# Performance work log

Hardware: AMD Instinct MI355X
Metric: run time of the kernel (lower is better)

## Reference

```python
import jax, jax.numpy as jnp
import numpy as np

DN = ('NCHW', 'OIHW', 'NCHW')

def conv(x, w, b=None, pad='SAME'):
    y = jax.lax.conv_general_dilated(x, w, (1, 1), pad, dimension_numbers=DN)
    if b is not None:
        y = y + b[None, :, None, None]
    return y

def prelu(x, a):
    return jnp.where(x >= 0, x, a * x)

def ca_layer(x, w_a, w_b):
    # global avg pool -> 1x1 conv -> relu -> 1x1 conv -> sigmoid -> gate
    g = jnp.mean(x, axis=(2, 3), keepdims=True)          # [B,C,1,1]
    g = jax.nn.relu(conv(g, w_a))
    g = jax.nn.sigmoid(conv(g, w_b))
    return x * g

def head(x, w, b, ca_a, ca_b):
    y = conv(x, w, b)                                    # [B,4,H,W]
    y = ca_layer(y, ca_a, ca_b)
    return jax.nn.softmax(y, axis=1)                     # Softmax2d = softmax over C

def box_kernel(k):
    return jnp.full((1, 1, k, k), 1.0 / (k * k), dtype=jnp.float32)

def multiscale_blur(x):
    # SAME-padded uniform box filters of sizes 1,5,15,25 on [B,1,H,W]
    return [x if k == 1 else conv(x, box_kernel(k)) for k in (1, 5, 15, 25)]

def weighted_combine(h, blurs):
    # h: [B,4,H,W] softmax weights; blurs: list of 4 [B,1,H,W]
    return sum(h[:, i:i+1] * blurs[i] for i in range(4))

def setup_inputs() -> dict:
    key = jax.random.key(0)
    ks = jax.random.split(key, 32)
    B, H, W = 8, 512, 512
    s = 0.05
    inp = {
        'x':  jax.random.normal(ks[0], (B, 1, H, W), jnp.float32),
        'w1': jax.random.normal(ks[1], (32, 1, 3, 3), jnp.float32) * s,
        'b1': jnp.zeros((32,), jnp.float32),
        'a1': jnp.float32(0.25),
        'w2': jax.random.normal(ks[2], (64, 32, 3, 3), jnp.float32) * s,
        'b2': jnp.zeros((64,), jnp.float32),
        'a2': jnp.float32(0.25),
        'w3': jax.random.normal(ks[3], (32, 64, 3, 3), jnp.float32) * s,
        'b3': jnp.zeros((32,), jnp.float32),
        'a3': jnp.float32(0.25),
    }
    for i, kk in zip((1, 2, 3), (4, 8, 12)):
        inp[f'hw{i}'] = jax.random.normal(ks[kk], (4, 32, 3, 3), jnp.float32) * s
        inp[f'hb{i}'] = jnp.zeros((4,), jnp.float32)
        inp[f'ca{i}a'] = jax.random.normal(ks[kk + 1], (4, 4, 1, 1), jnp.float32) * s
        inp[f'ca{i}b'] = jax.random.normal(ks[kk + 2], (4, 4, 1, 1), jnp.float32) * s
    return inp

def reference(x, w1, b1, a1, w2, b2, a2, w3, b3, a3,
              hw1, hb1, ca1a, ca1b, hw2, hb2, ca2a, ca2b, hw3, hb3, ca3a, ca3b):
    body = prelu(conv(x, w1, b1), a1)
    body = prelu(conv(body, w2, b2), a2)
    body = prelu(conv(body, w3, b3), a3)            # [B,32,H,W]
    h1 = head(body, hw1, hb1, ca1a, ca1b)
    h2 = head(body, hw2, hb2, ca2a, ca2b)
    h3 = head(body, hw3, hb3, ca3a, ca3b)
    out1 = weighted_combine(h1, multiscale_blur(x))
    out2 = weighted_combine(h2, multiscale_blur(out1))
    out3 = weighted_combine(h3, multiscale_blur(out2))
    return out3
```

## Files before the change

### kernel.cpp

```cpp
#include <hip/hip_runtime.h>

#define HH 512
#define WW 512
#define NB 8
#define HWSZ (HH * WW)
#define PW 516
#define PROWS 514

typedef float f32x4 __attribute__((ext_vector_type(4)));
typedef float f32x16 __attribute__((ext_vector_type(16)));
typedef short bf16x8 __attribute__((ext_vector_type(8)));

__device__ __forceinline__ unsigned short f2bf(float f) {
  union { float f; unsigned u; } v; v.f = f;
  unsigned r = v.u + 0x7FFFu + ((v.u >> 16) & 1u);
  return (unsigned short)(r >> 16);
}
__device__ __forceinline__ float bf2f(unsigned u16) {
  union { unsigned u; float f; } v; v.u = u16 << 16;
  return v.f;
}

__device__ __forceinline__ void gload16(const uint4* g, uint4* l) {
  __builtin_amdgcn_global_load_lds((__attribute__((address_space(1))) void*)g,
                                   (__attribute__((address_space(3))) void*)l, 16, 0, 0);
}

#define PS1 ((size_t)PROWS * PW * 32)
#define PS2 ((size_t)PROWS * PW * 64)
#define NZ1 (2 * 4 * PW * 8 + 512 * 4 * 16)
#define NZ2 (2 * 8 * PW * 8 + 512 * 8 * 16)

__device__ __forceinline__ void zp(unsigned short* buf, int NCH, int i) {
  int rowShorts = NCH * PW * 8;
  if (i < 2 * rowShorts) {
    size_t r = (i < rowShorts) ? 0 : 513;
    int j = i % rowShorts;
    buf[r * rowShorts + j] = 0;
    return;
  }
  i -= 2 * rowShorts;
  int perRow = NCH * 16;
  int r = 1 + i / perRow;
  int j = i % perRow;
  int ch = j >> 4;
  int c = (j & 8) ? 513 : 0;
  int e = j & 7;
  buf[(((size_t)r * NCH + ch) * PW + c) * 8 + e] = 0;
}

__global__ __launch_bounds__(256) void k_prep(const float* __restrict__ w2,
                                              const float* __restrict__ w3,
                                              const float* __restrict__ h0,
                                              const float* __restrict__ h1,
                                              const float* __restrict__ h2,
                                              unsigned short* __restrict__ wp2,
                                              unsigned short* __restrict__ wp3,
                                              unsigned short* __restrict__ wph,
                                              unsigned short* __restrict__ t1,
                                              unsigned short* __restrict__ t2,
                                              float* __restrict__ S) {
  int i = blockIdx.x * 256 + threadIdx.x;
  const int N1 = 9 * 64 * 32;
  const int N2 = N1 + 9 * 32 * 64;
  const int N3 = N2 + 9 * 16 * 32;
  const int N4 = N3 + 4 * NZ1;
  const int N5 = N4 + 4 * NZ2;
  const int N6 = N5 + 128;
  if (i < N1) {
    int j8 = i & 7;
    int lane = (i >> 3) & 63;
    int mt = (i >> 9) & 1;
    int ks = (i >> 10) & 1;
    int tap = i >> 11;
    int l31 = lane & 31, h16 = lane >> 5;
    int oc = mt * 32 + l31;
    int ic = ks * 16 + h16 * 8 + j8;
    wp2[i] = f2bf(w2[(oc * 32 + ic) * 9 + tap]);
  } else if (i < N2) {
    int j = i - N1;
    int ic = j & 63, t = j >> 6, oc = t & 31, k = t >> 5;
    wp3[j] = f2bf(w3[(oc * 64 + ic) * 9 + k]);
  } else if (i < N3) {
    int j = i - N2;
    int ic = j & 31, t = j >> 5, oc = t & 15, k = t >> 4;
    float v = 0.f;
    if (oc < 12) {
      const float* w = oc < 4 ? h0 : (oc < 8 ? h1 : h2);
      v = w[((oc & 3) * 32 + ic) * 9 + k];
    }
    wph[j] = f2bf(v);
  } else if (i < N4) {
    int j = i - N3;
    zp(t1 + (size_t)(j / NZ1) * PS1, 4, j % NZ1);
  } else if (i < N5) {
    int j = i - N4;
    zp(t2 + (size_t)(j / NZ2) * PS2, 8, j % NZ2);
  } else if (i < N6) {
    S[i - N5] = 0.f;
  }
}

__global__ __launch_bounds__(256) void k_conv1(const float* __restrict__ x,
                                               const float* __restrict__ w,
                                               const float* __restrict__ bias,
                                               const float* __restrict__ a_ptr,
                                               unsigned short* __restrict__ out) {
  const float* xp = x + (size_t)blockIdx.z * HWSZ;
  uint4* out4 = (uint4*)(out + (size_t)blockIdx.z * PS1);
  int pix = blockIdx.x * 256 + threadIdx.x;
  int h = pix >> 9, wc = pix & 511;
  float t[9];
#pragma unroll
  for (int dh = 0; dh < 3; dh++)
#pragma unroll
    for (int dw = 0; dw < 3; dw++) {
      int hh = h + dh - 1, ww = wc + dw - 1;
      t[dh * 3 + dw] =
          (hh >= 0 && hh < HH && ww >= 0 && ww < WW) ? xp[hh * WW + ww] : 0.f;
    }
  float a = a_ptr[0];
  unsigned pk[16];
#pragma unroll
  for (int oc = 0; oc < 32; oc++) {
    float s = bias[oc];
#pragma unroll
    for (int k = 0; k < 9; k++) s = fmaf(w[oc * 9 + k], t[k], s);
    s = s >= 0.f ? s : a * s;
    unsigned short b = f2bf(s);
    if (oc & 1)
      pk[oc >> 1] |= ((unsigned)b) << 16;
    else
      pk[oc >> 1] = b;
  }
#pragma unroll
  for (int q = 0; q < 4; q++)
    out4[((size_t)(h + 1) * 4 + q) * PW + (wc + 1)] = *(uint4*)&pk[q * 4];
}

__global__ __launch_bounds__(256, 2) void k_convm2(const unsigned short* __restrict__ in,
                                                   const unsigned short* __restrict__ wp,
                                                   const float* __restrict__ bias,
                                                   const float* __restrict__ a_ptr,
                                                   unsigned short* __restrict__ out) {
  __shared__ __align__(16) short ring[10 * 4 * 68 * 8];
  __shared__ __align__(16) short wlds[9 * 2 * 2 * 64 * 8];
  const int tid = threadIdx.x, lane = tid & 63, wid = tid >> 6;
  const int l31 = lane & 31, h16 = lane >> 5;
  const int c0 = blockIdx.x * 64;
  const int R0 = blockIdx.y * 32;
  const uint4* in4 = (const uint4*)(in + (size_t)blockIdx.z * PS1);
  unsigned short* outz = out + (size_t)blockIdx.z * PS2;
  uint4* ring4 = (uint4*)ring;
  uint4* wl4 = (uint4*)wlds;
  const uint4* wp4 = (const uint4*)wp;

  for (int sg = wid; sg < 36; sg += 4)
    gload16(wp4 + sg * 64 + lane, wl4 + sg * 64);

  auto load_rows = [&](int rfirst, int nrows) {
    int nseg = nrows * 4;
    for (int sg = wid; sg < nseg; sg += 4) {
      int rr = rfirst + (sg >> 2);
      int ch = sg & 3;
      const uint4* src = in4 + (size_t)(rr * 4 + ch) * PW + c0;
      uint4* dst = ring4 + ((rr % 10) * 4 + ch) * 68;
      gload16(src + lane, dst);
      gload16(src + 4 + lane, dst + 4);
    }
  };

  const float alpha = a_ptr[0];
  load_rows(R0, 6);

  for (int k = 0; k < 8; ++k) {
    const int rb = R0 + 4 * k;
    __syncthreads();
    if (k < 7) load_rows(rb + 6, 4);

    f32x16 acc[2][2];
#pragma unroll
    for (int nt = 0; nt < 2; nt++)
#pragma unroll
      for (int mt = 0; mt < 2; mt++)
#pragma unroll
        for (int j = 0; j < 16; j++) acc[nt][mt][j] = 0.f;

#pragma unroll
    for (int dh = 0; dh < 3; dh++) {
      bf16x8 af[3][2][2];
#pragma unroll
      for (int dw = 0; dw < 3; dw++)
#pragma unroll
        for (int ks = 0; ks < 2; ks++)
#pragma unroll
          for (int mt = 0; mt < 2; mt++)
            af[dw][ks][mt] = *(const bf16x8*)(
                wlds + ((((size_t)((dh * 3 + dw) * 2 + ks) * 2 + mt) * 64 + lane) * 8));
      const short* lrow = ring + (size_t)(((rb + wid + dh) % 10) * 4) * 68 * 8;
#pragma unroll
      for (int dw = 0; dw < 3; dw++) {
        const int pl0 = l31 + dw, pl1 = 32 + l31 + dw;
#pragma unroll
        for (int ks = 0; ks < 2; ks++) {
          const int blk = ks * 2 + h16;
          bf16x8 b0 = *(const bf16x8*)(lrow + (blk * 68 + pl0) * 8);
          bf16x8 b1 = *(const bf16x8*)(lrow + (blk * 68 + pl1) * 8);
#pragma unroll
          for (int mt = 0; mt < 2; mt++)
            acc[0][mt] = __builtin_amdgcn_mfma_f32_32x32x16_bf16(af[dw][ks][mt],
                                                                 b0, acc[0][mt], 0, 0, 0);
#pragma unroll
          for (int mt = 0; mt < 2; mt++)
            acc[1][mt] = __builtin_amdgcn_mfma_f32_32x32x16_bf16(af[dw][ks][mt],
                                                                 b1, acc[1][mt], 0, 0, 0);
        }
      }
    }

    const int orow = rb + wid + 1;
    uint2* o2 = (uint2*)outz;
#pragma unroll
    for (int nt = 0; nt < 2; nt++) {
      const int ocol = c0 + nt * 32 + l31 + 1;
#pragma unroll
      for (int mt = 0; mt < 2; mt++)
#pragma unroll
        for (int g = 0; g < 4; g++) {
          int oc0 = mt * 32 + g * 8 + h16 * 4;
          f32x4 bv = *(const f32x4*)(bias + oc0);
          float v[4];
#pragma unroll
          for (int j = 0; j < 4; j++) {
            float s = acc[nt][mt][g * 4 + j] + bv[j];
            v[j] = s >= 0.f ? s : alpha * s;
          }
          uint2 pk;
          pk.x = (unsigned)f2bf(v[0]) | ((unsigned)f2bf(v[1]) << 16);
          pk.y = (unsigned)f2bf(v[2]) | ((unsigned)f2bf(v[3]) << 16);
          size_t idx16 = ((size_t)orow * 8 + (mt * 4 + g)) * PW + ocol;
          o2[idx16 * 2 + h16] = pk;
        }
    }
  }
}

__global__ __launch_bounds__(256, 2) void k_convm3(const unsigned short* __restrict__ in,
                                                   const unsigned short* __restrict__ wp,
                                                   const float* __restrict__ bias,
                                                   const float* __restrict__ a_ptr,
                                                   unsigned short* __restrict__ out) {
  __shared__ __align__(16) short lds[8 * 8 * 68 * 8];
  const int tid = threadIdx.x, lane = tid & 63, wid = tid >> 6;
  const int l31 = lane & 31, h16 = lane >> 5;
  const int c0 = blockIdx.x * 64;
  const int R0 = blockIdx.y * 32;
  const uint4* in4 = (const uint4*)(in + (size_t)blockIdx.z * PS2);
  unsigned short* outz = out + (size_t)blockIdx.z * PS1;
  uint4* lds4 = (uint4*)lds;

  bf16x8 af[9][4];
#pragma unroll
  for (int k9 = 0; k9 < 9; k9++)
#pragma unroll
    for (int ks = 0; ks < 4; ks++)
      af[k9][ks] = *(const bf16x8*)(
          wp + ((size_t)(k9 * 32 + l31) * 64 + ks * 16 + h16 * 8));

  auto load_rows = [&](int rfirst, int nrows) {
    int nseg = nrows * 8;
    for (int sg = wid; sg < nseg; sg += 4) {
      int rr = rfirst + (sg >> 3);
      int ch = sg & 7;
      const uint4* src = in4 + (size_t)(rr * 8 + ch) * PW + c0;
      uint4* dst = lds4 + ((rr & 7) * 8 + ch) * 68;
      gload16(src + lane, dst);
      gload16(src + 4 + lane, dst + 4);
    }
  };

  const float alpha = a_ptr[0];
  load_rows(R0, 6);

  for (int k = 0; k < 8; ++k) {
    const int rb = R0 + 4 * k;
    __syncthreads();
    if (k < 7) load_rows(rb + 6, 2);

    f32x16 acc[2];
#pragma unroll
    for (int nt = 0; nt < 2; nt++)
#pragma unroll
      for (int j = 0; j < 16; j++) acc[nt][j] = 0.f;

#pragma unroll
    for (int dh = 0; dh < 3; dh++) {
      const short* lrow = lds + (size_t)(((rb + wid + dh) & 7) * 8) * 68 * 8;
#pragma unroll
      for (int dw = 0; dw < 3; dw++) {
        const int pl0 = l31 + dw, pl1 = 32 + l31 + dw;
#pragma unroll
        for (int ks = 0; ks < 4; ks++) {
          const int blk = ks * 2 + h16;
          bf16x8 b0 = *(const bf16x8*)(lrow + (blk * 68 + pl0) * 8);
          bf16x8 b1 = *(const bf16x8*)(lrow + (blk * 68 + pl1) * 8);
          acc[0] = __builtin_amdgcn_mfma_f32_32x32x16_bf16(af[dh * 3 + dw][ks],
                                                           b0, acc[0], 0, 0, 0);
          acc[1] = __builtin_amdgcn_mfma_f32_32x32x16_bf16(af[dh * 3 + dw][ks],
                                                           b1, acc[1], 0, 0, 0);
        }
      }
    }

    const int orow = rb + wid + 1;
    uint2* o2 = (uint2*)outz;
#pragma unroll
    for (int nt = 0; nt < 2; nt++) {
      const int ocol = c0 + nt * 32 + l31 + 1;
#pragma unroll
      for (int g = 0; g < 4; g++) {
        int oc0 = g * 8 + h16 * 4;
        f32x4 bv = *(const f32x4*)(bias + oc0);
        float v[4];
#pragma unroll
        for (int j = 0; j < 4; j++) {
          float s = acc[nt][g * 4 + j] + bv[j];
          v[j] = s >= 0.f ? s : alpha * s;
        }
        uint2 pk;
        pk.x = (unsigned)f2bf(v[0]) | ((unsigned)f2bf(v[1]) << 16);
        pk.y = (unsigned)f2bf(v[2]) | ((unsigned)f2bf(v[3]) << 16);
        size_t idx16 = ((size_t)orow * 4 + g) * PW + ocol;
        o2[idx16 * 2 + h16] = pk;
      }
    }
    __syncthreads();
    if (k < 7) load_rows(rb + 8, 2);
  }
}

__global__ __launch_bounds__(256, 2) void k_headm(const unsigned short* __restrict__ in,
                                                  const unsigned short* __restrict__ wp,
                                                  const float* __restrict__ hb0,
                                                  const float* __restrict__ hb1,
                                                  const float* __restrict__ hb2,
                                                  unsigned short* __restrict__ pre,
                                                  float* __restrict__ S) {
  __shared__ __align__(16) short lds[8 * 4 * 68 * 8];
  __shared__ float part[4][4][4];
  const int tid = threadIdx.x, lane = tid & 63, wid = tid >> 6;
  const int l15 = lane & 15, q = lane >> 4;
  const int c0 = blockIdx.x * 64;
  const int R0 = blockIdx.y * 32;
  const uint4* in4 = (const uint4*)(in + (size_t)blockIdx.z * PS1);
  float* Sz = S + blockIdx.z * 16;
  uint4* lds4 = (uint4*)lds;

  bf16x8 af[9];
#pragma unroll
  for (int k9 = 0; k9 < 9; k9++)
    af[k9] = *(const bf16x8*)(wp + (size_t)(k9 * 16 + l15) * 32 + q * 8);

  float bs[4];
#pragma unroll
  for (int r = 0; r < 4; r++) {
    int oc = q * 4 + r;
    bs[r] = oc < 4 ? hb0[oc] : (oc < 8 ? hb1[oc - 4] : (oc < 12 ? hb2[oc - 8] : 0.f));
  }
  unsigned short* prehq = pre + ((size_t)(q * 4 + blockIdx.z) * HWSZ) * 4;

  auto load_rows = [&](int rfirst, int nrows) {
    int nseg = nrows * 4;
    for (int sg = wid; sg < nseg; sg += 4) {
      int rr = rfirst + (sg >> 2);
      int ch = sg & 3;
      const uint4* src = in4 + (size_t)(rr * 4 + ch) * PW + c0;
      uint4* dst = lds4 + ((rr & 7) * 4 + ch) * 68;
      gload16(src + lane, dst);
      gload16(src + 4 + lane, dst + 4);
    }
  };

  load_rows(R0, 6);
  float csum[4] = {0.f, 0.f, 0.f, 0.f};

  for (int k = 0; k < 8; ++k) {
    const int rb = R0 + 4 * k;
    __syncthreads();
    if (k < 7) load_rows(rb + 6, 2);

    f32x4 acc[4];
#pragma unroll
    for (int nt = 0; nt < 4; nt++)
#pragma unroll
      for (int j = 0; j < 4; j++) acc[nt][j] = 0.f;

#pragma unroll
    for (int dh = 0; dh < 3; dh++) {
      const short* lrow = lds + (size_t)(((rb + wid + dh) & 7) * 4) * 68 * 8;
#pragma unroll
      for (int dw = 0; dw < 3; dw++) {
        bf16x8 a = af[dh * 3 + dw];
#pragma unroll
        for (int nt = 0; nt < 4; nt++) {
          int pl = nt * 16 + l15 + dw;
          bf16x8 b = *(const bf16x8*)(lrow + (q * 68 + pl) * 8);
          acc[nt] = __builtin_amdgcn_mfma_f32_16x16x32_bf16(a, b, acc[nt], 0, 0, 0);
        }
      }
    }

    const int orow = rb + wid;
#pragma unroll
    for (int nt = 0; nt < 4; nt++) {
      int pix = orow * 512 + c0 + nt * 16 + l15;
      float v[4];
#pragma unroll
      for (int r = 0; r < 4; r++) {
        v[r] = acc[nt][r] + bs[r];
        csum[r] += v[r];
      }
      uint2 pk;
      pk.x = (unsigned)f2bf(v[0]) | ((unsigned)f2bf(v[1]) << 16);
      pk.y = (unsigned)f2bf(v[2]) | ((unsigned)f2bf(v[3]) << 16);
      *(uint2*)(prehq + (size_t)pix * 4) = pk;
    }
    __syncthreads();
    if (k < 7) load_rows(rb + 8, 2);
  }

#pragma unroll
  for (int d = 1; d < 16; d <<= 1)
#pragma unroll
    for (int r = 0; r < 4; r++) csum[r] += __shfl_xor(csum[r], d, 64);
  if (l15 == 0)
#pragma unroll
    for (int r = 0; r < 4; r++) part[wid][q][r] = csum[r];
  __syncthreads();
  if (tid < 12) {
    int oc = tid;
    float s = part[0][oc >> 2][oc & 3] + part[1][oc >> 2][oc & 3] +
              part[2][oc >> 2][oc & 3] + part[3][oc >> 2][oc & 3];
    atomicAdd(&Sz[oc], s);
  }
}

#define BT 32
#define RAD 12
#define SRCT (BT + 2 * RAD)
__global__ __launch_bounds__(256) void k_blurcombine(const float* __restrict__ src,
                                                     const unsigned short* __restrict__ preh,
                                                     const float* __restrict__ S4,
                                                     const float* __restrict__ wa,
                                                     const float* __restrict__ wb,
                                                     float* __restrict__ dst) {
  __shared__ float tile[SRCT][SRCT];
  __shared__ float hs[3][SRCT][BT];
  __shared__ float g[4];
  const float* srcz = src + (size_t)blockIdx.z * HWSZ;
  const unsigned short* prez = preh + (size_t)blockIdx.z * HWSZ * 4;
  const float* S4z = S4 + blockIdx.z * 16;
  float* dstz = dst + (size_t)blockIdx.z * HWSZ;
  int h0 = blockIdx.y * BT - RAD, w0 = blockIdx.x * BT - RAD;
  if (threadIdx.x < 4) {
    int o = threadIdx.x;
    float m[4], ga[4];
#pragma unroll
    for (int c = 0; c < 4; c++) m[c] = S4z[c] * (1.0f / (float)HWSZ);
#pragma unroll
    for (int c = 0; c < 4; c++) {
      float s = 0.f;
#pragma unroll
      for (int j = 0; j < 4; j++) s = fmaf(wa[c * 4 + j], m[j], s);
      ga[c] = fmaxf(s, 0.f);
    }
    float s2 = 0.f;
#pragma unroll
    for (int c = 0; c < 4; c++) s2 = fmaf(wb[o * 4 + c], ga[c], s2);
    g[o] = 1.f / (1.f + expf(-s2));
  }
  for (int idx = threadIdx.x; idx < SRCT * SRCT; idx += 256) {
    int r = idx / SRCT, c = idx % SRCT;
    int hh = h0 + r, ww = w0 + c;
    float v = 0.f;
    if (hh >= 0 && hh < HH && ww >= 0 && ww < WW) v = srcz[hh * WW + ww];
    tile[r][c] = v;
  }
  __syncthreads();
  for (int idx = threadIdx.x; idx < SRCT * BT; idx += 256) {
    int r = idx / BT, j = idx % BT;
    int cc = j + RAD;
    float s5 = 0.f;
#pragma unroll
    for (int d = -2; d <= 2; d++) s5 += tile[r][cc + d];
    float s15 = s5;
#pragma unroll
    for (int d = 3; d <= 7; d++) s15 += tile[r][cc + d] + tile[r][cc - d];
    float s25 = s15;
#pragma unroll
    for (int d = 8; d <= 12; d++) s25 += tile[r][cc + d] + tile[r][cc - d];
    hs[0][r][j] = s5;
    hs[1][r][j] = s15;
    hs[2][r][j] = s25;
  }
  __syncthreads();
  for (int p = threadIdx.x; p < BT * BT; p += 256) {
    int i = p / BT, j = p % BT;
    int rr = i + RAD;
    float b1 = 0.f;
#pragma unroll
    for (int d = -2; d <= 2; d++) b1 += hs[0][rr + d][j];
    float b2 = 0.f;
#pragma unroll
    for (int d = -7; d <= 7; d++) b2 += hs[1][rr + d][j];
    float b3 = 0.f;
#pragma unroll
    for (int d = -12; d <= 12; d++) b3 += hs[2][rr + d][j];
    b1 *= (1.f / 25.f);
    b2 *= (1.f / 225.f);
    b3 *= (1.f / 625.f);
    float b0 = tile[rr][j + RAD];
    int y = blockIdx.y * BT + i, x = blockIdx.x * BT + j;
    int pix = y * WW + x;
    uint2 pk = *(const uint2*)(prez + (size_t)pix * 4);
    float v[4];
    v[0] = bf2f(pk.x & 0xffffu) * g[0];
    v[1] = bf2f(pk.x >> 16) * g[1];
    v[2] = bf2f(pk.y & 0xffffu) * g[2];
    v[3] = bf2f(pk.y >> 16) * g[3];
    float mx = fmaxf(fmaxf(v[0], v[1]), fmaxf(v[2], v[3]));
    float e0 = expf(v[0] - mx), e1 = expf(v[1] - mx), e2 = expf(v[2] - mx),
          e3 = expf(v[3] - mx);
    float inv = 1.f / (e0 + e1 + e2 + e3);
    dstz[pix] = (e0 * b0 + e1 * b1 + e2 * b2 + e3 * b3) * inv;
  }
}

extern "C" void kernel_launch(void* const* d_in, const int* in_sizes, int n_in,
                              void* d_out, int out_size, void* d_ws, size_t ws_size,
                              hipStream_t stream) {
  const float* x = (const float*)d_in[0];
  const float* w1 = (const float*)d_in[1];
  const float* b1 = (const float*)d_in[2];
  const float* a1 = (const float*)d_in[3];
  const float* w2 = (const float*)d_in[4];
  const float* b2 = (const float*)d_in[5];
  const float* a2 = (const float*)d_in[6];
  const float* w3 = (const float*)d_in[7];
  const float* b3 = (const float*)d_in[8];
  const float* a3 = (const float*)d_in[9];
  const float* hw[3] = {(const float*)d_in[10], (const float*)d_in[14], (const float*)d_in[18]};
  const float* hb[3] = {(const float*)d_in[11], (const float*)d_in[15], (const float*)d_in[19]};
  const float* caa[3] = {(const float*)d_in[12], (const float*)d_in[16], (const float*)d_in[20]};
  const float* cab[3] = {(const float*)d_in[13], (const float*)d_in[17], (const float*)d_in[21]};

  char* base = (char*)d_ws;
  size_t off = 0;
  auto alloc = [&](size_t bytes) {
    char* p = base + off;
    off = (off + bytes + 63) & ~(size_t)63;
    return p;
  };
  unsigned short* t1 = (unsigned short*)alloc(4 * PS1 * 2);
  unsigned short* t2 = (unsigned short*)alloc(4 * PS2 * 2);
  unsigned short* pre = (unsigned short*)alloc(16 * (size_t)HWSZ * 4 * 2);
  unsigned short* wp2 = (unsigned short*)alloc(9 * 64 * 32 * 2);
  unsigned short* wp3 = (unsigned short*)alloc(9 * 64 * 32 * 2);
  unsigned short* wph = (unsigned short*)alloc(9 * 16 * 32 * 2);
  float* out1 = (float*)alloc(4 * (size_t)HWSZ * 4);
  float* out2 = (float*)alloc(4 * (size_t)HWSZ * 4);
  float* S = (float*)alloc(8 * 16 * 4);

  dim3 blk(256);
  {
    int total = 9 * 64 * 32 + 9 * 32 * 64 + 9 * 16 * 32 + 4 * NZ1 + 4 * NZ2 + 128;
    k_prep<<<(total + 255) / 256, blk, 0, stream>>>(w2, w3, hw[0], hw[1], hw[2], wp2,
                                                    wp3, wph, t1, t2, S);
  }

  dim3 gc1(1024, 1, 4);
  dim3 gconv(8, 16, 4);
  dim3 gbc(WW / BT, HH / BT, 4);
  const size_t preplane = (size_t)HWSZ * 4;
  for (int g = 0; g < 2; g++) {
    const float* xg = x + (size_t)g * 4 * HWSZ;
    float* Sg = S + g * 64;
    float* outg = (float*)d_out + (size_t)g * 4 * HWSZ;
    k_conv1<<<gc1, blk, 0, stream>>>(xg, w1, b1, a1, t1);
    k_convm2<<<gconv, blk, 0, stream>>>(t1, wp2, b2, a2, t2);
    k_convm3<<<gconv, blk, 0, stream>>>(t2, wp3, b3, a3, t1);
    k_headm<<<gconv, blk, 0, stream>>>(t1, wph, hb[0], hb[1], hb[2], pre, Sg);
    k_blurcombine<<<gbc, blk, 0, stream>>>(xg, pre + 0 * 4 * preplane, Sg + 0, caa[0], cab[0], out1);
    k_blurcombine<<<gbc, blk, 0, stream>>>(out1, pre + 1 * 4 * preplane, Sg + 4, caa[1], cab[1], out2);
    k_blurcombine<<<gbc, blk, 0, stream>>>(out2, pre + 2 * 4 * preplane, Sg + 8, caa[2], cab[2], outg);
  }
}
```

Baseline: 480.5 us.

## Stage conv3 weights in LDS and halve column tile to cut registers

The third conv kernel no longer keeps all 36 weight fragments in registers. It stages the prepacked weights in shared memory via global_load_lds and reloads 12 fragments per kernel row. The column tile shrinks from 64 to 32, with one accumulator instead of two and a grid doubled in x, and the weight prepack is reordered into a lane-major MFMA fragment layout. The aim is lower register pressure and more blocks in flight, at the cost of extra LDS reads, more halo reloading per output and less weight reuse per block.

```diff
diff --git a/kernel.cpp b/kernel.cpp
--- a/kernel.cpp
+++ b/kernel.cpp
@@ -79,8 +79,13 @@
     wp2[i] = f2bf(w2[(oc * 32 + ic) * 9 + tap]);
   } else if (i < N2) {
     int j = i - N1;
-    int ic = j & 63, t = j >> 6, oc = t & 31, k = t >> 5;
-    wp3[j] = f2bf(w3[(oc * 64 + ic) * 9 + k]);
+    int j8 = j & 7;
+    int lane = (j >> 3) & 63;
+    int ks = (j >> 9) & 3;
+    int tap = j >> 11;
+    int l31 = lane & 31, h16 = lane >> 5;
+    int ic = ks * 16 + h16 * 8 + j8;
+    wp3[j] = f2bf(w3[(l31 * 64 + ic) * 9 + tap]);
   } else if (i < N3) {
     int j = i - N2;
     int ic = j & 31, t = j >> 5, oc = t & 15, k = t >> 4;
@@ -250,22 +255,20 @@
                                                    const float* __restrict__ bias,
                                                    const float* __restrict__ a_ptr,
                                                    unsigned short* __restrict__ out) {
-  __shared__ __align__(16) short lds[8 * 8 * 68 * 8];
+  __shared__ __align__(16) short ring[8 * 8 * 36 * 8];
+  __shared__ __align__(16) short wlds[9 * 4 * 64 * 8];
   const int tid = threadIdx.x, lane = tid & 63, wid = tid >> 6;
   const int l31 = lane & 31, h16 = lane >> 5;
-  const int c0 = blockIdx.x * 64;
+  const int c0 = blockIdx.x * 32;
   const int R0 = blockIdx.y * 32;
   const uint4* in4 = (const uint4*)(in + (size_t)blockIdx.z * PS2);
   unsigned short* outz = out + (size_t)blockIdx.z * PS1;
-  uint4* lds4 = (uint4*)lds;
-
-  bf16x8 af[9][4];
-#pragma unroll
-  for (int k9 = 0; k9 < 9; k9++)
-#pragma unroll
-    for (int ks = 0; ks < 4; ks++)
-      af[k9][ks] = *(const bf16x8*)(
-          wp + ((size_t)(k9 * 32 + l31) * 64 + ks * 16 + h16 * 8));
+  uint4* ring4 = (uint4*)ring;
+  uint4* wl4 = (uint4*)wlds;
+  const uint4* wp4 = (const uint4*)wp;
+
+  for (int sg = wid; sg < 36; sg += 4)
+    gload16(wp4 + sg * 64 + lane, wl4 + sg * 64);
 
   auto load_rows = [&](int rfirst, int nrows) {
     int nseg = nrows * 8;
@@ -273,9 +276,8 @@
       int rr = rfirst + (sg >> 3);
       int ch = sg & 7;
       const uint4* src = in4 + (size_t)(rr * 8 + ch) * PW + c0;
-      uint4* dst = lds4 + ((rr & 7) * 8 + ch) * 68;
-      gload16(src + lane, dst);
-      gload16(src + 4 + lane, dst + 4);
+      uint4* dst = ring4 + ((rr & 7) * 8 + ch) * 36;
+      if (lane < 36) gload16(src + lane, dst);
     }
   };
 
@@ -287,52 +289,50 @@
     __syncthreads();
     if (k < 7) load_rows(rb + 6, 2);
 
-    f32x16 acc[2];
-#pragma unroll
-    for (int nt = 0; nt < 2; nt++)
-#pragma unroll
-      for (int j = 0; j < 16; j++) acc[nt][j] = 0.f;
+    f32x16 acc;
+#pragma unroll
+    for (int j = 0; j < 16; j++) acc[j] = 0.f;
 
 #pragma unroll
     for (int dh = 0; dh < 3; dh++) {
-      const short* lrow = lds + (size_t)(((rb + wid + dh) & 7) * 8) * 68 * 8;
+      bf16x8 af[3][4];
+#pragma unroll
+      for (int dw = 0; dw < 3; dw++)
+#pragma unroll
+        for (int ks = 0; ks < 4; ks++)
+          af[dw][ks] = *(const bf16x8*)(
+              wlds + (((size_t)((dh * 3 + dw) * 4 + ks) * 64 + lane) * 8));
+      const short* lrow = ring + (size_t)(((rb + wid + dh) & 7) * 8) * 36 * 8;
 #pragma unroll
       for (int dw = 0; dw < 3; dw++) {
-        const int pl0 = l31 + dw, pl1 = 32 + l31 + dw;
+        const int pl = l31 + dw;
 #pragma unroll
         for (int ks = 0; ks < 4; ks++) {
           const int blk = ks * 2 + h16;
-          bf16x8 b0 = *(const bf16x8*)(lrow + (blk * 68 + pl0) * 8);
-          bf16x8 b1 = *(const bf16x8*)(lrow + (blk * 68 + pl1) * 8);
-          acc[0] = __builtin_amdgcn_mfma_f32_32x32x16_bf16(af[dh * 3 + dw][ks],
-                                                           b0, acc[0], 0, 0, 0);
-          acc[1] = __builtin_amdgcn_mfma_f32_32x32x16_bf16(af[dh * 3 + dw][ks],
-                                                           b1, acc[1], 0, 0, 0);
+          bf16x8 b = *(const bf16x8*)(lrow + (blk * 36 + pl) * 8);
+          acc = __builtin_amdgcn_mfma_f32_32x32x16_bf16(af[dw][ks], b, acc, 0, 0, 0);
         }
       }
     }
 
     const int orow = rb + wid + 1;
+    const int ocol = c0 + l31 + 1;
     uint2* o2 = (uint2*)outz;
 #pragma unroll
-    for (int nt = 0; nt < 2; nt++) {
-      const int ocol = c0 + nt * 32 + l31 + 1;
-#pragma unroll
-      for (int g = 0; g < 4; g++) {
-        int oc0 = g * 8 + h16 * 4;
-        f32x4 bv = *(const f32x4*)(bias + oc0);
-        float v[4];
-#pragma unroll
-        for (int j = 0; j < 4; j++) {
-          float s = acc[nt][g * 4 + j] + bv[j];
-          v[j] = s >= 0.f ? s : alpha * s;
-        }
-        uint2 pk;
-        pk.x = (unsigned)f2bf(v[0]) | ((unsigned)f2bf(v[1]) << 16);
-        pk.y = (unsigned)f2bf(v[2]) | ((unsigned)f2bf(v[3]) << 16);
-        size_t idx16 = ((size_t)orow * 4 + g) * PW + ocol;
-        o2[idx16 * 2 + h16] = pk;
+    for (int g = 0; g < 4; g++) {
+      int oc0 = g * 8 + h16 * 4;
+      f32x4 bv = *(const f32x4*)(bias + oc0);
+      float v[4];
+#pragma unroll
+      for (int j = 0; j < 4; j++) {
+        float s = acc[g * 4 + j] + bv[j];
+        v[j] = s >= 0.f ? s : alpha * s;
       }
+      uint2 pk;
+      pk.x = (unsigned)f2bf(v[0]) | ((unsigned)f2bf(v[1]) << 16);
+      pk.y = (unsigned)f2bf(v[2]) | ((unsigned)f2bf(v[3]) << 16);
+      size_t idx16 = ((size_t)orow * 4 + g) * PW + ocol;
+      o2[idx16 * 2 + h16] = pk;
     }
     __syncthreads();
     if (k < 7) load_rows(rb + 8, 2);
@@ -580,6 +580,7 @@
 
   dim3 gc1(1024, 1, 4);
   dim3 gconv(8, 16, 4);
+  dim3 gconv3(16, 16, 4);
   dim3 gbc(WW / BT, HH / BT, 4);
   const size_t preplane = (size_t)HWSZ * 4;
   for (int g = 0; g < 2; g++) {
@@ -588,7 +589,7 @@
     float* outg = (float*)d_out + (size_t)g * 4 * HWSZ;
     k_conv1<<<gc1, blk, 0, stream>>>(xg, w1, b1, a1, t1);
     k_convm2<<<gconv, blk, 0, stream>>>(t1, wp2, b2, a2, t2);
-    k_convm3<<<gconv, blk, 0, stream>>>(t2, wp3, b3, a3, t1);
+    k_convm3<<<gconv3, blk, 0, stream>>>(t2, wp3, b3, a3, t1);
     k_headm<<<gconv, blk, 0, stream>>>(t1, wph, hb[0], hb[1], hb[2], pre, Sg);
     k_blurcombine<<<gbc, blk, 0, stream>>>(xg, pre + 0 * 4 * preplane, Sg + 0, caa[0], cab[0], out1);
     k_blurcombine<<<gbc, blk, 0, stream>>>(out1, pre + 1 * 4 * preplane, Sg + 4, caa[1], cab[1], out2);
```

Result: faster. 468.6 us (-2.5%).
